# Kernel tuning notes

Hardware: AMD Instinct MI355X
Metric: run time of the kernel (lower is better)

## Reference

```python
import jax, jax.numpy as jnp
import numpy as np
import math

D_MODEL = 512
N_HEADS = 8
D_K = D_MODEL // N_HEADS
D_FF = 2048
EPS = 1e-6


def _layer_norm(x, gamma, beta):
    # Matches the torch module: unbiased std (ddof=1), divide by (std + eps)
    mean = jnp.mean(x, axis=-1, keepdims=True)
    std = jnp.std(x, axis=-1, ddof=1, keepdims=True)
    return gamma * (x - mean) / (std + EPS) + beta


def setup_inputs() -> dict:
    key = jax.random.key(0)
    ks = jax.random.split(key, 16)
    B, S = 4, 2048
    s_attn = 1.0 / math.sqrt(D_MODEL)
    s_ff1 = 1.0 / math.sqrt(D_MODEL)
    s_ff2 = 1.0 / math.sqrt(D_FF)
    inp = {
        "x": jax.random.normal(ks[0], (B, S, D_MODEL), dtype=jnp.float32),
        "mask": jnp.ones((1, 1, S, S), dtype=jnp.int32),
        "wq": jax.random.normal(ks[1], (D_MODEL, D_MODEL), jnp.float32) * s_attn,
        "bq": jnp.zeros((D_MODEL,), jnp.float32),
        "wk": jax.random.normal(ks[2], (D_MODEL, D_MODEL), jnp.float32) * s_attn,
        "bk": jnp.zeros((D_MODEL,), jnp.float32),
        "wv": jax.random.normal(ks[3], (D_MODEL, D_MODEL), jnp.float32) * s_attn,
        "bv": jnp.zeros((D_MODEL,), jnp.float32),
        "wo": jax.random.normal(ks[4], (D_MODEL, D_MODEL), jnp.float32) * s_attn,
        "bo": jnp.zeros((D_MODEL,), jnp.float32),
        "w1": jax.random.normal(ks[5], (D_MODEL, D_FF), jnp.float32) * s_ff1,
        "b1": jnp.zeros((D_FF,), jnp.float32),
        "w2": jax.random.normal(ks[6], (D_FF, D_MODEL), jnp.float32) * s_ff2,
        "b2": jnp.zeros((D_MODEL,), jnp.float32),
        "g1": jnp.ones((1, 1, D_MODEL), jnp.float32),
        "be1": jnp.zeros((1, 1, D_MODEL), jnp.float32),
        "g2": jnp.ones((1, 1, D_MODEL), jnp.float32),
        "be2": jnp.zeros((1, 1, D_MODEL), jnp.float32),
    }
    return inp


def reference(x, mask, wq, bq, wk, bk, wv, bv, wo, bo, w1, b1, w2, b2, g1, be1, g2, be2):
    B, S, _ = x.shape
    # --- residual 1: pre-norm self-attention ---
    xn = _layer_norm(x, g1, be1)
    q = (xn @ wq + bq).reshape(B, S, N_HEADS, D_K).transpose(0, 2, 1, 3)
    k = (xn @ wk + bk).reshape(B, S, N_HEADS, D_K).transpose(0, 2, 1, 3)
    v = (xn @ wv + bv).reshape(B, S, N_HEADS, D_K).transpose(0, 2, 1, 3)
    # NOTE: source uses floor division `//` by sqrt(d_k) (a faithful-ly kept bug)
    scores = jnp.floor_divide(jnp.einsum("bhqd,bhkd->bhqk", q, k), math.sqrt(D_K))
    scores = jnp.where(mask == 0, jnp.float32(-1e9), scores)
    attn = jax.nn.softmax(scores, axis=-1)
    ctx = jnp.einsum("bhqk,bhkd->bhqd", attn, v)
    ctx = ctx.transpose(0, 2, 1, 3).reshape(B, S, D_MODEL)
    x = x + (ctx @ wo + bo)
    # --- residual 2: pre-norm feed-forward ---
    xn2 = _layer_norm(x, g2, be2)
    ff = jax.nn.relu(xn2 @ w1 + b1) @ w2 + b2
    return x + ff
```

## Files before the change

### kernel.cpp

```cpp
#include <hip/hip_runtime.h>
#include <cmath>

#define SEQ 2048
#define DM 512
#define DFF 2048
#define NH 8
#define DKH 64
#define NROWS 8192

typedef __attribute__((ext_vector_type(8))) short bf16x8;
typedef __attribute__((ext_vector_type(16))) float f32x16;

__device__ __forceinline__ ushort f2bf(float f) {
    uint u = __float_as_uint(f);
    u += 0x7fff + ((u >> 16) & 1);
    return (ushort)(u >> 16);
}
__device__ __forceinline__ float bf2f(ushort h) {
    return __uint_as_float(((uint)h) << 16);
}
__device__ __forceinline__ uint cvtpk_bf16(float a, float b) {
    uint r;
    asm("v_cvt_pk_bf16_f32 %0, %1, %2" : "=v"(r) : "v"(a), "v"(b));
    return r;
}
__device__ __forceinline__ void gl_lds16(const void* g, void* l) {
    __builtin_amdgcn_global_load_lds(
        (const __attribute__((address_space(1))) void*)g,
        (__attribute__((address_space(3))) void*)l, 16, 0, 0);
}
__device__ __forceinline__ void* swz(char* base, int row, int col) {
    int byte = (row << 7) + (col << 1);
    byte ^= (row & 7) << 4;
    return base + byte;
}
__device__ __forceinline__ void* swzg(char* base, int row, int k) {
    int byte = (row << 7) + (k << 1);
    byte ^= ((row >> 2) & 7) << 4;
    return base + byte;
}

template<bool SPLIT>
__global__ __launch_bounds__(64) void ln_kernel(const float* __restrict__ x,
        const float* __restrict__ g, const float* __restrict__ b,
        ushort* __restrict__ oh, ushort* __restrict__ ol) {
    int row = blockIdx.x;
    int t = threadIdx.x;
    const float* xr = x + (size_t)row * DM + t * 8;
    float v[8];
    *(float4*)&v[0] = *(const float4*)(xr);
    *(float4*)&v[4] = *(const float4*)(xr + 4);
    float s = 0.f;
    #pragma unroll
    for (int j = 0; j < 8; ++j) s += v[j];
    #pragma unroll
    for (int m = 32; m > 0; m >>= 1) s += __shfl_xor(s, m);
    float mean = s * (1.0f / DM);
    float ss = 0.f;
    #pragma unroll
    for (int j = 0; j < 8; ++j) { float d = v[j] - mean; ss += d * d; }
    #pragma unroll
    for (int m = 32; m > 0; m >>= 1) ss += __shfl_xor(ss, m);
    float inv = 1.0f / (sqrtf(ss * (1.0f / (DM - 1))) + 1e-6f);
    float gv[8], bv[8];
    *(float4*)&gv[0] = *(const float4*)(g + t * 8);
    *(float4*)&gv[4] = *(const float4*)(g + t * 8 + 4);
    *(float4*)&bv[0] = *(const float4*)(b + t * 8);
    *(float4*)&bv[4] = *(const float4*)(b + t * 8 + 4);
    union { ushort us[8]; float4 f4; } ph, pl;
    #pragma unroll
    for (int j = 0; j < 8; ++j) {
        float o = gv[j] * (v[j] - mean) * inv + bv[j];
        ushort hb = f2bf(o);
        ph.us[j] = hb;
        if (SPLIT) pl.us[j] = f2bf(o - bf2f(hb));
    }
    *(float4*)(oh + (size_t)row * DM + t * 8) = ph.f4;
    if (SPLIT) *(float4*)(ol + (size_t)row * DM + t * 8) = pl.f4;
}

__global__ __launch_bounds__(256) void wconv4(
        const float* __restrict__ wq, const float* __restrict__ wk,
        const float* __restrict__ wv, const float* __restrict__ wo,
        ushort* __restrict__ qh, ushort* __restrict__ ql,
        ushort* __restrict__ kh, ushort* __restrict__ kl,
        ushort* __restrict__ vh, ushort* __restrict__ oh) {
    const int K = DM, N = DM;
    __shared__ float tile[64][65];
    int z = blockIdx.z;
    const float* W = (z == 0) ? wq : (z == 1) ? wk : (z == 2) ? wv : wo;
    ushort* Th = (z == 0) ? qh : (z == 1) ? kh : (z == 2) ? vh : oh;
    ushort* Tl = (z == 0) ? ql : (z == 1) ? kl : nullptr;
    bool split = (z < 2);
    int k0 = blockIdx.x * 64, n0 = blockIdx.y * 64;
    int t = threadIdx.x;
    {
        int kr = t >> 2, c0 = (t & 3) * 16;
        const float* src = W + (size_t)(k0 + kr) * N + n0 + c0;
        #pragma unroll
        for (int j = 0; j < 4; ++j)
            *(float4*)&tile[kr][c0 + j * 4] = *(const float4*)(src + j * 4);
    }
    __syncthreads();
    int n = t >> 2, kc = (t & 3) * 16;
    union { ushort us[16]; float4 f4[2]; } ph, pl;
    #pragma unroll
    for (int j = 0; j < 16; ++j) {
        float v = tile[kc + j][n];
        ushort hb = f2bf(v);
        ph.us[j] = hb;
        pl.us[j] = f2bf(v - bf2f(hb));
    }
    ushort* dh = Th + (size_t)(n0 + n) * K + k0 + kc;
    *(float4*)(dh) = ph.f4[0];
    *(float4*)(dh + 8) = ph.f4[1];
    if (split) {
        ushort* dl = Tl + (size_t)(n0 + n) * K + k0 + kc;
        *(float4*)(dl) = pl.f4[0];
        *(float4*)(dl + 8) = pl.f4[1];
    }
}

__global__ __launch_bounds__(256) void wconv(const float* __restrict__ W,
        ushort* __restrict__ Th, int K, int N) {
    __shared__ float tile[64][65];
    int k0 = blockIdx.x * 64, n0 = blockIdx.y * 64;
    int t = threadIdx.x;
    {
        int kr = t >> 2, c0 = (t & 3) * 16;
        const float* src = W + (size_t)(k0 + kr) * N + n0 + c0;
        #pragma unroll
        for (int j = 0; j < 4; ++j)
            *(float4*)&tile[kr][c0 + j * 4] = *(const float4*)(src + j * 4);
    }
    __syncthreads();
    int n = t >> 2, kc = (t & 3) * 16;
    union { ushort us[16]; float4 f4[2]; } ph;
    #pragma unroll
    for (int j = 0; j < 16; ++j) ph.us[j] = f2bf(tile[kc + j][n]);
    ushort* dh = Th + (size_t)(n0 + n) * K + k0 + kc;
    *(float4*)(dh) = ph.f4[0];
    *(float4*)(dh + 8) = ph.f4[1];
}

__global__ __launch_bounds__(256) void vtrans(const ushort* __restrict__ vh,
        ushort* __restrict__ vt) {
    __shared__ __align__(16) char tile[8192];
    int s0 = blockIdx.x * 64;
    int bh = blockIdx.y;
    int b = bh >> 3, h = bh & 7;
    int t = threadIdx.x;
    {
        int r = t >> 2, co = (t & 3) * 16;
        const ushort* src = vh + (size_t)(b * SEQ + s0 + r) * DM + h * DKH + co;
        *(float4*)swz(tile, r, co) = *(const float4*)(src);
        *(float4*)swz(tile, r, co + 8) = *(const float4*)(src + 8);
    }
    __syncthreads();
    int d = t >> 2, j0 = (t & 3) * 16;
    union { ushort us[16]; float4 f4[2]; } o;
    #pragma unroll
    for (int j = 0; j < 16; ++j)
        o.us[j] = *(ushort*)swz(tile, j0 + j, d);
    ushort* dst = vt + ((size_t)bh * DKH + d) * SEQ + s0 + j0;
    *(float4*)(dst) = o.f4[0];
    *(float4*)(dst + 8) = o.f4[1];
}

__global__ __launch_bounds__(64) void maskprep(const int* __restrict__ mask,
        ushort* __restrict__ mb, unsigned char* __restrict__ mflag) {
    int row = blockIdx.x;
    int lane = threadIdx.x;
    ushort neg = f2bf(-1e9f);
    unsigned long long bal[4];
    #pragma unroll
    for (int u = 0; u < 4; ++u) {
        int base = row * SEQ + u * 512 + lane * 8;
        int4 a = *(const int4*)(mask + base);
        int4 c = *(const int4*)(mask + base + 4);
        union { ushort us[8]; float4 f4; } o;
        o.us[0] = a.x ? (ushort)0 : neg;
        o.us[1] = a.y ? (ushort)0 : neg;
        o.us[2] = a.z ? (ushort)0 : neg;
        o.us[3] = a.w ? (ushort)0 : neg;
        o.us[4] = c.x ? (ushort)0 : neg;
        o.us[5] = c.y ? (ushort)0 : neg;
        o.us[6] = c.z ? (ushort)0 : neg;
        o.us[7] = c.w ? (ushort)0 : neg;
        *(float4*)(mb + base) = o.f4;
        bool ok = a.x && a.y && a.z && a.w && c.x && c.y && c.z && c.w;
        bal[u] = __ballot(ok);
    }
    if (lane < 32) {
        int u = lane >> 3;
        unsigned long long bsel = bal[0];
        bsel = (u == 1) ? bal[1] : bsel;
        bsel = (u == 2) ? bal[2] : bsel;
        bsel = (u == 3) ? bal[3] : bsel;
        int byte = (int)((bsel >> ((lane & 7) * 8)) & 0xFFull);
        mflag[row * 32 + lane] = (byte == 0xFF) ? 1 : 0;
    }
}

template<bool RELU, bool HASRES, int OUT>
__global__ __launch_bounds__(256) void mgemm(
        const ushort* __restrict__ Ah, const ushort* __restrict__ Bth,
        const float* __restrict__ bias, const float* __restrict__ resid,
        float* __restrict__ Cf, ushort* __restrict__ Cbh,
        int M, int N, int K) {
    __shared__ __align__(16) char smem[65536];
    int tid = threadIdx.x;
    int lane = tid & 63, w = tid >> 6;
    int ln31 = lane & 31, hi = lane >> 5;
    int mh = (w >> 1) * 64, nh = (w & 1) * 64;
    int gx = gridDim.x;
    int nwg = gx * gridDim.y;
    int flat = blockIdx.y * gx + blockIdx.x;
    int sid = (flat & 7) * (nwg >> 3) + (flat >> 3);
    int n0 = (sid % gx) * 128;
    int m0 = (sid / gx) * 128;

    f32x16 acc[2][2];
    #pragma unroll
    for (int i = 0; i < 2; ++i)
        #pragma unroll
        for (int j = 0; j < 2; ++j)
            #pragma unroll
            for (int r = 0; r < 16; ++r) acc[i][j][r] = 0.f;

    auto stage = [&](char* Abuf, char* Bbuf, int k0) {
        #pragma unroll
        for (int c = 0; c < 4; ++c) {
            int ch = w * 4 + c;
            int r = ch * 8 + (lane >> 3);
            int u = (lane & 7) ^ ((r >> 2) & 7);
            gl_lds16(Ah + (size_t)(m0 + r) * K + k0 + u * 8, Abuf + ch * 1024);
            gl_lds16(Bth + (size_t)(n0 + r) * K + k0 + u * 8, Bbuf + ch * 1024);
        }
    };

    char* A0 = smem;
    char* B0 = smem + 16384;
    char* A1 = smem + 32768;
    char* B1 = smem + 49152;

    stage(A0, B0, 0);
    __syncthreads();
    int nk = K / 64;
    for (int kt = 0; kt < nk; ++kt) {
        char* Ac = (kt & 1) ? A1 : A0;
        char* Bc = (kt & 1) ? B1 : B0;
        if (kt + 1 < nk)
            stage((kt & 1) ? A0 : A1, (kt & 1) ? B0 : B1, (kt + 1) * 64);
        __builtin_amdgcn_s_setprio(1);
        #pragma unroll
        for (int km = 0; km < 4; ++km) {
            int kk = km * 16 + hi * 8;
            bf16x8 ah[2], bh[2];
            ah[0] = *(bf16x8*)swzg(Ac, mh + ln31, kk);
            ah[1] = *(bf16x8*)swzg(Ac, mh + 32 + ln31, kk);
            bh[0] = *(bf16x8*)swzg(Bc, nh + ln31, kk);
            bh[1] = *(bf16x8*)swzg(Bc, nh + 32 + ln31, kk);
            #pragma unroll
            for (int mi = 0; mi < 2; ++mi)
                #pragma unroll
                for (int ni = 0; ni < 2; ++ni)
                    acc[mi][ni] = __builtin_amdgcn_mfma_f32_32x32x16_bf16(
                        ah[mi], bh[ni], acc[mi][ni], 0, 0, 0);
        }
        __builtin_amdgcn_s_setprio(0);
        __syncthreads();
    }
    float bv[2];
    bv[0] = bias[n0 + nh + ln31];
    bv[1] = bias[n0 + nh + 32 + ln31];
    #pragma unroll
    for (int mi = 0; mi < 2; ++mi)
        #pragma unroll
        for (int ni = 0; ni < 2; ++ni) {
            int n = n0 + nh + ni * 32 + ln31;
            #pragma unroll
            for (int r = 0; r < 16; ++r) {
                int m = m0 + mh + mi * 32 + (r & 3) + 8 * (r >> 2) + 4 * hi;
                float v = acc[mi][ni][r] + bv[ni];
                if (HASRES) v += resid[(size_t)m * N + n];
                if (RELU) v = fmaxf(v, 0.f);
                size_t idx = (size_t)m * N + n;
                if (OUT == 0) Cf[idx] = v;
                else Cbh[idx] = f2bf(v);
            }
        }
}

__global__ __launch_bounds__(256) void qkv_gemm(
        const ushort* __restrict__ Ah, const ushort* __restrict__ Al,
        const ushort* __restrict__ Bth, const ushort* __restrict__ Btl,
        const float* __restrict__ bq, const float* __restrict__ bk,
        const float* __restrict__ bv_, ushort* __restrict__ q_h,
        ushort* __restrict__ q_l, ushort* __restrict__ k_h,
        ushort* __restrict__ k_l, ushort* __restrict__ v_h) {
    const int K = DM, N = DM;
    __shared__ __align__(16) char smem[65536];
    char* As_h = smem;
    char* Bs_h = smem + 16384;
    char* As_l = smem + 32768;
    char* Bs_l = smem + 49152;
    int tid = threadIdx.x;
    int lane = tid & 63, w = tid >> 6;
    int ln31 = lane & 31, hi = lane >> 5;
    int mh = (w >> 1) * 64, nh = (w & 1) * 64;
    int gx = gridDim.x;
    int nwg = gx * gridDim.y;
    int flat = blockIdx.y * gx + blockIdx.x;
    int sid = (flat & 7) * (nwg >> 3) + (flat >> 3);
    int n0 = (sid % gx) * 128;
    int m0 = (sid / gx) * 128;
    bool isqk = (n0 < 1024);

    f32x16 acc[2][2];
    #pragma unroll
    for (int i = 0; i < 2; ++i)
        #pragma unroll
        for (int j = 0; j < 2; ++j)
            #pragma unroll
            for (int r = 0; r < 16; ++r) acc[i][j][r] = 0.f;

    for (int k0 = 0; k0 < K; k0 += 64) {
        #pragma unroll
        for (int c = 0; c < 4; ++c) {
            int ch = w * 4 + c;
            int r = ch * 8 + (lane >> 3);
            int u = (lane & 7) ^ ((r >> 2) & 7);
            gl_lds16(Ah + (size_t)(m0 + r) * K + k0 + u * 8, As_h + ch * 1024);
            gl_lds16(Bth + (size_t)(n0 + r) * K + k0 + u * 8, Bs_h + ch * 1024);
            if (isqk) {
                gl_lds16(Al + (size_t)(m0 + r) * K + k0 + u * 8, As_l + ch * 1024);
                gl_lds16(Btl + (size_t)(n0 + r) * K + k0 + u * 8, Bs_l + ch * 1024);
            }
        }
        __syncthreads();
        __builtin_amdgcn_s_setprio(1);
        #pragma unroll
        for (int km = 0; km < 4; ++km) {
            int kk = km * 16 + hi * 8;
            bf16x8 ah[2], bh[2];
            ah[0] = *(bf16x8*)swzg(As_h, mh + ln31, kk);
            ah[1] = *(bf16x8*)swzg(As_h, mh + 32 + ln31, kk);
            bh[0] = *(bf16x8*)swzg(Bs_h, nh + ln31, kk);
            bh[1] = *(bf16x8*)swzg(Bs_h, nh + 32 + ln31, kk);
            if (isqk) {
                bf16x8 al[2], bl[2];
                al[0] = *(bf16x8*)swzg(As_l, mh + ln31, kk);
                al[1] = *(bf16x8*)swzg(As_l, mh + 32 + ln31, kk);
                bl[0] = *(bf16x8*)swzg(Bs_l, nh + ln31, kk);
                bl[1] = *(bf16x8*)swzg(Bs_l, nh + 32 + ln31, kk);
                #pragma unroll
                for (int mi = 0; mi < 2; ++mi)
                    #pragma unroll
                    for (int ni = 0; ni < 2; ++ni) {
                        acc[mi][ni] = __builtin_amdgcn_mfma_f32_32x32x16_bf16(
                            ah[mi], bh[ni], acc[mi][ni], 0, 0, 0);
                        acc[mi][ni] = __builtin_amdgcn_mfma_f32_32x32x16_bf16(
                            ah[mi], bl[ni], acc[mi][ni], 0, 0, 0);
                        acc[mi][ni] = __builtin_amdgcn_mfma_f32_32x32x16_bf16(
                            al[mi], bh[ni], acc[mi][ni], 0, 0, 0);
                    }
            } else {
                #pragma unroll
                for (int mi = 0; mi < 2; ++mi)
                    #pragma unroll
                    for (int ni = 0; ni < 2; ++ni)
                        acc[mi][ni] = __builtin_amdgcn_mfma_f32_32x32x16_bf16(
                            ah[mi], bh[ni], acc[mi][ni], 0, 0, 0);
            }
        }
        __builtin_amdgcn_s_setprio(0);
        __syncthreads();
    }
    const float* bias = (n0 < 512) ? bq : (n0 < 1024 ? bk : bv_);
    int ncol0 = n0 & 511;
    ushort* Oh = (n0 < 512) ? q_h : (n0 < 1024 ? k_h : v_h);
    ushort* Ol = (n0 < 512) ? q_l : (n0 < 1024 ? k_l : nullptr);
    float bvv[2];
    bvv[0] = bias[ncol0 + nh + ln31];
    bvv[1] = bias[ncol0 + nh + 32 + ln31];
    #pragma unroll
    for (int mi = 0; mi < 2; ++mi)
        #pragma unroll
        for (int ni = 0; ni < 2; ++ni) {
            int n = ncol0 + nh + ni * 32 + ln31;
            #pragma unroll
            for (int r = 0; r < 16; ++r) {
                int m = m0 + mh + mi * 32 + (r & 3) + 8 * (r >> 2) + 4 * hi;
                float v = acc[mi][ni][r] + bvv[ni];
                size_t idx = (size_t)m * N + n;
                ushort hb = f2bf(v);
                Oh[idx] = hb;
                if (isqk) Ol[idx] = f2bf(v - bf2f(hb));
            }
        }
}

__global__ __launch_bounds__(256, 3) void attn_kernel(
        const ushort* __restrict__ Qh, const ushort* __restrict__ Ql,
        const ushort* __restrict__ Khg, const ushort* __restrict__ Klg,
        const ushort* __restrict__ Vtg, const ushort* __restrict__ mb,
        const unsigned char* __restrict__ mflag,
        ushort* __restrict__ pctx0, ushort* __restrict__ pctx1,
        float2* __restrict__ ml) {
    __shared__ __align__(16) char smem[49152];
    int tid = threadIdx.x;
    int w = tid >> 6, lane = tid & 63;
    int ln31 = lane & 31, hi = lane >> 5;
    bool hib = (hi != 0);
    int f = blockIdx.y * gridDim.x + blockIdx.x;
    int g = (f & 7) * 128 + (f >> 3);
    int bh = g >> 5, rest = g & 31;
    int part = rest >> 4, qb = rest & 15;
    int b = bh >> 3, h = bh & 7;
    int q0 = qb * 128;
    size_t brow = (size_t)b * SEQ;
    int hcol = h * DKH;
    int ktbeg = part * 16, ktend = ktbeg + 16;

    auto stage_kv = [&](char* buf, int kt) {
        #pragma unroll
        for (int c = 0; c < 2; ++c) {
            int ch = w * 2 + c;
            int r = ch * 8 + (lane >> 3);
            int u = (lane & 7) ^ (r & 7);
            gl_lds16(Khg + (brow + kt * 64 + r) * DM + hcol + u * 8,
                     buf + ch * 1024);
            gl_lds16(Klg + (brow + kt * 64 + r) * DM + hcol + u * 8,
                     buf + 8192 + ch * 1024);
            gl_lds16(Vtg + ((size_t)bh * DKH + r) * SEQ + kt * 64 + u * 8,
                     buf + 16384 + ch * 1024);
        }
    };

    {
        char* QhL = smem;
        char* QlL = smem + 16384;
        #pragma unroll
        for (int c = 0; c < 4; ++c) {
            int ch = w * 4 + c;
            int r = ch * 8 + (lane >> 3);
            int u = (lane & 7) ^ (r & 7);
            gl_lds16(Qh + (brow + q0 + r) * DM + hcol + u * 8, QhL + ch * 1024);
            gl_lds16(Ql + (brow + q0 + r) * DM + hcol + u * 8, QlL + ch * 1024);
        }
    }
    __syncthreads();
    bf16x8 qfh[4], qfl[4];
    {
        int qr = w * 32 + ln31;
        #pragma unroll
        for (int c = 0; c < 4; ++c) {
            qfh[c] = *(bf16x8*)swz(smem, qr, c * 16 + hi * 8);
            qfl[c] = *(bf16x8*)swz(smem + 16384, qr, c * 16 + hi * 8);
        }
    }
    __syncthreads();
    stage_kv(smem + (ktbeg & 1) * 24576, ktbeg);
    __syncthreads();

    f32x16 ctx0, ctx1;
    #pragma unroll
    for (int r = 0; r < 16; ++r) { ctx0[r] = 0.f; ctx1[r] = 0.f; }
    float m_i = -1e30f, l_i = 0.f;
    int qglob = q0 + w * 32 + ln31;
    const ushort* mrow = mb + (size_t)qglob * SEQ;

    for (int kt = ktbeg; kt < ktend; ++kt) {
        char* cur = smem + (kt & 1) * 24576;
        if (kt + 1 < ktend)
            stage_kv(smem + ((kt + 1) & 1) * 24576, kt + 1);
        unsigned char fl = mflag[qglob * 32 + kt];
        bool domask = !__all(fl != 0);
        ushort4 mpre[8];
        if (domask) {
            #pragma unroll
            for (int i = 0; i < 8; ++i)
                mpre[i] = *(const ushort4*)(mrow + kt * 64 + i * 8 + hi * 4);
        }
        char* KhL = cur;
        char* KlL = cur + 8192;
        char* VtL = cur + 16384;
        #pragma unroll
        for (int ksub = 0; ksub < 2; ++ksub) {
            f32x16 s;
            #pragma unroll
            for (int r = 0; r < 16; ++r) s[r] = 0.f;
            __builtin_amdgcn_s_setprio(1);
            #pragma unroll
            for (int c = 0; c < 4; ++c) {
                bf16x8 ka = *(bf16x8*)swz(KhL, ksub * 32 + ln31, c * 16 + hi * 8);
                bf16x8 kb = *(bf16x8*)swz(KlL, ksub * 32 + ln31, c * 16 + hi * 8);
                s = __builtin_amdgcn_mfma_f32_32x32x16_bf16(ka, qfh[c], s, 0, 0, 0);
                s = __builtin_amdgcn_mfma_f32_32x32x16_bf16(ka, qfl[c], s, 0, 0, 0);
                s = __builtin_amdgcn_mfma_f32_32x32x16_bf16(kb, qfh[c], s, 0, 0, 0);
            }
            __builtin_amdgcn_s_setprio(0);
            float tmax = -1e30f;
            if (domask) {
                #pragma unroll
                for (int rg = 0; rg < 4; ++rg) {
                    ushort4 mv = mpre[ksub * 4 + rg];
                    ushort mu[4] = {mv.x, mv.y, mv.z, mv.w};
                    #pragma unroll
                    for (int j = 0; j < 4; ++j) {
                        int r = rg * 4 + j;
                        float sc = floorf(s[r] * 0.125f) + bf2f(mu[j]);
                        s[r] = sc;
                        tmax = fmaxf(tmax, sc);
                    }
                }
            } else {
                #pragma unroll
                for (int r = 0; r < 16; ++r) {
                    float sc = floorf(s[r] * 0.125f);
                    s[r] = sc;
                    tmax = fmaxf(tmax, sc);
                }
            }
            tmax = fmaxf(tmax, __shfl_xor(tmax, 32));
            if (!__all(tmax <= m_i)) {
                float newm = fmaxf(m_i, tmax);
                float scl = __expf(m_i - newm);
                m_i = newm;
                l_i *= scl;
                #pragma unroll
                for (int r = 0; r < 16; ++r) { ctx0[r] *= scl; ctx1[r] *= scl; }
            }
            float psum = 0.f;
            #pragma unroll
            for (int r = 0; r < 16; ++r) {
                float p = __expf(s[r] - m_i);
                s[r] = p;
                psum += p;
            }
            psum += __shfl_xor(psum, 32);
            l_i += psum;
            uint pk0[4], pk1[4];
            #pragma unroll
            for (int rg = 0; rg < 4; ++rg) {
                pk0[rg] = cvtpk_bf16(s[rg * 4 + 0], s[rg * 4 + 1]);
                pk1[rg] = cvtpk_bf16(s[rg * 4 + 2], s[rg * 4 + 3]);
            }
            __builtin_amdgcn_s_setprio(1);
            #pragma unroll
            for (int cc = 0; cc < 2; ++cc) {
                uint A0 = pk0[cc * 2], A1 = pk1[cc * 2];
                uint B0 = pk0[cc * 2 + 1], B1 = pk1[cc * 2 + 1];
                uint send0 = hib ? A0 : B0;
                uint send1 = hib ? A1 : B1;
                uint own0  = hib ? B0 : A0;
                uint own1  = hib ? B1 : A1;
                uint recv0 = (uint)__shfl_xor((int)send0, 32);
                uint recv1 = (uint)__shfl_xor((int)send1, 32);
                union { uint u[4]; bf16x8 v; } pb;
                pb.u[0] = hib ? recv0 : own0;
                pb.u[1] = hib ? recv1 : own1;
                pb.u[2] = hib ? own0 : recv0;
                pb.u[3] = hib ? own1 : recv1;
                int c = ksub * 2 + cc;
                bf16x8 va0 = *(bf16x8*)swz(VtL, ln31, c * 16 + hi * 8);
                bf16x8 va1 = *(bf16x8*)swz(VtL, 32 + ln31, c * 16 + hi * 8);
                ctx0 = __builtin_amdgcn_mfma_f32_32x32x16_bf16(va0, pb.v, ctx0, 0, 0, 0);
                ctx1 = __builtin_amdgcn_mfma_f32_32x32x16_bf16(va1, pb.v, ctx1, 0, 0, 0);
            }
            __builtin_amdgcn_s_setprio(0);
        }
        __syncthreads();
    }

    ushort* P = part ? pctx1 : pctx0;
    size_t pbase = ((size_t)bh * SEQ + qglob) * DKH;
    #pragma unroll
    for (int r = 0; r < 16; ++r) {
        int d = (r & 3) + 8 * (r >> 2) + 4 * hi;
        P[pbase + d] = f2bf(ctx0[r]);
        P[pbase + 32 + d] = f2bf(ctx1[r]);
    }
    if (hi == 0)
        ml[((size_t)part * 32 + bh) * SEQ + qglob] = make_float2(m_i, l_i);
}

__global__ __launch_bounds__(256) void attn_combine(
        const ushort* __restrict__ p0, const ushort* __restrict__ p1,
        const float2* __restrict__ ml, ushort* __restrict__ O) {
    int idx = blockIdx.x * 256 + threadIdx.x;
    int d0 = (idx & 7) * 8;
    int q = (idx >> 3) & (SEQ - 1);
    int bh = idx >> 14;
    int b = bh >> 3, h = bh & 7;
    size_t pb = ((size_t)bh * SEQ + q) * DKH + d0;
    bf16x8 c0 = *(const bf16x8*)(p0 + pb);
    bf16x8 c1 = *(const bf16x8*)(p1 + pb);
    float2 e0 = ml[(size_t)bh * SEQ + q];
    float2 e1 = ml[((size_t)32 + bh) * SEQ + q];
    float m = fmaxf(e0.x, e1.x);
    float w0 = __expf(e0.x - m), w1 = __expf(e1.x - m);
    float inv = 1.0f / (e0.y * w0 + e1.y * w1);
    union { ushort us[8]; float4 f4; } o;
    #pragma unroll
    for (int j = 0; j < 8; ++j) {
        float v0 = bf2f((ushort)c0[j]);
        float v1 = bf2f((ushort)c1[j]);
        o.us[j] = f2bf((v0 * w0 + v1 * w1) * inv);
    }
    *(float4*)(O + ((size_t)(b * SEQ + q)) * DM + h * DKH + d0) = o.f4;
}

extern "C" void kernel_launch(void* const* d_in, const int* in_sizes, int n_in,
                              void* d_out, int out_size, void* d_ws, size_t ws_size,
                              hipStream_t stream) {
    const float* x    = (const float*)d_in[0];
    const int*   mask = (const int*)d_in[1];
    const float* wq = (const float*)d_in[2];
    const float* bq = (const float*)d_in[3];
    const float* wk = (const float*)d_in[4];
    const float* bk = (const float*)d_in[5];
    const float* wv = (const float*)d_in[6];
    const float* bv = (const float*)d_in[7];
    const float* wo = (const float*)d_in[8];
    const float* bo = (const float*)d_in[9];
    const float* w1 = (const float*)d_in[10];
    const float* b1 = (const float*)d_in[11];
    const float* w2 = (const float*)d_in[12];
    const float* b2 = (const float*)d_in[13];
    const float* g1  = (const float*)d_in[14];
    const float* be1 = (const float*)d_in[15];
    const float* g2  = (const float*)d_in[16];
    const float* be2 = (const float*)d_in[17];
    float* out = (float*)d_out;

    char* ws = (char*)d_ws;
    const size_t MiB = 1024 * 1024;
    ushort* xn_h = (ushort*)(ws);
    ushort* xn_l = (ushort*)(ws + 8 * MiB);
    ushort* q_h  = (ushort*)(ws + 16 * MiB);
    ushort* q_l  = (ushort*)(ws + 24 * MiB);
    ushort* k_h  = (ushort*)(ws + 32 * MiB);
    ushort* k_l  = (ushort*)(ws + 40 * MiB);
    ushort* v_h  = (ushort*)(ws + 48 * MiB);
    ushort* v_t  = (ushort*)(ws + 56 * MiB);
    ushort* wqkvt_h = (ushort*)(ws + 64 * MiB);
    ushort* wqkvt_l = (ushort*)(ws + 66 * MiB);
    ushort* wot_h = (ushort*)(ws + 67 * MiB);
    unsigned char* mflag = (unsigned char*)(ws + 67 * MiB + 512 * 1024);
    ushort* w1t_h = (ushort*)(ws + 68 * MiB);
    ushort* w2t_h = (ushort*)(ws + 70 * MiB);
    ushort* mb    = (ushort*)(ws + 72 * MiB);
    ushort* pctx0 = (ushort*)(ws + 80 * MiB);
    ushort* pctx1 = (ushort*)(ws + 88 * MiB);
    float2* ml    = (float2*)(ws + 64 * MiB);
    ushort* ctx  = xn_h;
    ushort* xn2  = xn_l;
    ushort* ff1  = q_h;

    dim3 blk256(256);
    wconv4<<<dim3(8, 8, 4), blk256, 0, stream>>>(
        wq, wk, wv, wo, wqkvt_h, wqkvt_l, wqkvt_h + 512 * 512,
        wqkvt_l + 512 * 512, wqkvt_h + 1024 * 512, wot_h);
    wconv<<<dim3(8, 32), blk256, 0, stream>>>(w1, w1t_h, DM, DFF);
    wconv<<<dim3(32, 8), blk256, 0, stream>>>(w2, w2t_h, DFF, DM);
    maskprep<<<SEQ, 64, 0, stream>>>(mask, mb, mflag);
    ln_kernel<true><<<NROWS, 64, 0, stream>>>(x, g1, be1, xn_h, xn_l);
    qkv_gemm<<<dim3(12, NROWS / 128), blk256, 0, stream>>>(
        xn_h, xn_l, wqkvt_h, wqkvt_l, bq, bk, bv, q_h, q_l, k_h, k_l, v_h);
    vtrans<<<dim3(SEQ / 64, 4 * NH), blk256, 0, stream>>>(v_h, v_t);
    {
        dim3 grid(32, 32);
        attn_kernel<<<grid, blk256, 0, stream>>>(
            q_h, q_l, k_h, k_l, v_t, mb, mflag, pctx0, pctx1, ml);
    }
    attn_combine<<<32 * SEQ * 8 / 256, blk256, 0, stream>>>(pctx0, pctx1, ml, ctx);
    {
        dim3 grid(DM / 128, NROWS / 128);
        mgemm<false,true,0><<<grid, blk256, 0, stream>>>(
            ctx, wot_h, bo, x, out, nullptr, NROWS, DM, DM);
    }
    ln_kernel<false><<<NROWS, 64, 0, stream>>>(out, g2, be2, xn2, nullptr);
    {
        dim3 grid(DFF / 128, NROWS / 128);
        mgemm<true,false,1><<<grid, blk256, 0, stream>>>(
            xn2, w1t_h, b1, nullptr, nullptr, ff1, NROWS, DFF, DM);
    }
    {
        dim3 grid(DM / 128, NROWS / 128);
        mgemm<false,true,0><<<grid, blk256, 0, stream>>>(
            ff1, w2t_h, b2, out, out, nullptr, NROWS, DM, DFF);
    }
}
```

Baseline: 238.2 us.

## Single-buffer V, widen QK tile, and fold score scale into Q projection

```diff
diff --git a/kernel.cpp b/kernel.cpp
--- a/kernel.cpp
+++ b/kernel.cpp
@@ -381,6 +381,7 @@
     int ncol0 = n0 & 511;
     ushort* Oh = (n0 < 512) ? q_h : (n0 < 1024 ? k_h : v_h);
     ushort* Ol = (n0 < 512) ? q_l : (n0 < 1024 ? k_l : nullptr);
+    float scale = (n0 < 512) ? 0.125f : 1.0f;
     float bvv[2];
     bvv[0] = bias[ncol0 + nh + ln31];
     bvv[1] = bias[ncol0 + nh + 32 + ln31];
@@ -392,7 +393,7 @@
             #pragma unroll
             for (int r = 0; r < 16; ++r) {
                 int m = m0 + mh + mi * 32 + (r & 3) + 8 * (r >> 2) + 4 * hi;
-                float v = acc[mi][ni][r] + bvv[ni];
+                float v = (acc[mi][ni][r] + bvv[ni]) * scale;
                 size_t idx = (size_t)m * N + n;
                 ushort hb = f2bf(v);
                 Oh[idx] = hb;
@@ -401,14 +402,14 @@
         }
 }
 
-__global__ __launch_bounds__(256, 3) void attn_kernel(
+__global__ __launch_bounds__(256, 4) void attn_kernel(
         const ushort* __restrict__ Qh, const ushort* __restrict__ Ql,
         const ushort* __restrict__ Khg, const ushort* __restrict__ Klg,
         const ushort* __restrict__ Vtg, const ushort* __restrict__ mb,
         const unsigned char* __restrict__ mflag,
         ushort* __restrict__ pctx0, ushort* __restrict__ pctx1,
         float2* __restrict__ ml) {
-    __shared__ __align__(16) char smem[49152];
+    __shared__ __align__(16) char smem[40960];
     int tid = threadIdx.x;
     int w = tid >> 6, lane = tid & 63;
     int ln31 = lane & 31, hi = lane >> 5;
@@ -423,7 +424,8 @@
     int hcol = h * DKH;
     int ktbeg = part * 16, ktend = ktbeg + 16;
 
-    auto stage_kv = [&](char* buf, int kt) {
+    auto stage_K = [&](int kt) {
+        char* buf = smem + (kt & 1) * 16384;
         #pragma unroll
         for (int c = 0; c < 2; ++c) {
             int ch = w * 2 + c;
@@ -433,8 +435,17 @@
                      buf + ch * 1024);
             gl_lds16(Klg + (brow + kt * 64 + r) * DM + hcol + u * 8,
                      buf + 8192 + ch * 1024);
+        }
+    };
+    auto stage_V = [&](int kt) {
+        char* buf = smem + 32768;
+        #pragma unroll
+        for (int c = 0; c < 2; ++c) {
+            int ch = w * 2 + c;
+            int r = ch * 8 + (lane >> 3);
+            int u = (lane & 7) ^ (r & 7);
             gl_lds16(Vtg + ((size_t)bh * DKH + r) * SEQ + kt * 64 + u * 8,
-                     buf + 16384 + ch * 1024);
+                     buf + ch * 1024);
         }
     };
 
@@ -461,7 +472,8 @@
         }
     }
     __syncthreads();
-    stage_kv(smem + (ktbeg & 1) * 24576, ktbeg);
+    stage_K(ktbeg);
+    stage_V(ktbeg);
     __syncthreads();
 
     f32x16 ctx0, ctx1;
@@ -472,82 +484,87 @@
     const ushort* mrow = mb + (size_t)qglob * SEQ;
 
     for (int kt = ktbeg; kt < ktend; ++kt) {
-        char* cur = smem + (kt & 1) * 24576;
-        if (kt + 1 < ktend)
-            stage_kv(smem + ((kt + 1) & 1) * 24576, kt + 1);
+        if (kt + 1 < ktend) stage_K(kt + 1);
+        char* KhL = smem + (kt & 1) * 16384;
+        char* KlL = KhL + 8192;
+        char* VtL = smem + 32768;
         unsigned char fl = mflag[qglob * 32 + kt];
         bool domask = !__all(fl != 0);
-        ushort4 mpre[8];
+
+        f32x16 s0, s1;
+        #pragma unroll
+        for (int r = 0; r < 16; ++r) { s0[r] = 0.f; s1[r] = 0.f; }
+        __builtin_amdgcn_s_setprio(1);
+        #pragma unroll
+        for (int c = 0; c < 4; ++c) {
+            bf16x8 ka0 = *(bf16x8*)swz(KhL, ln31, c * 16 + hi * 8);
+            bf16x8 kb0 = *(bf16x8*)swz(KlL, ln31, c * 16 + hi * 8);
+            bf16x8 ka1 = *(bf16x8*)swz(KhL, 32 + ln31, c * 16 + hi * 8);
+            bf16x8 kb1 = *(bf16x8*)swz(KlL, 32 + ln31, c * 16 + hi * 8);
+            s0 = __builtin_amdgcn_mfma_f32_32x32x16_bf16(ka0, qfh[c], s0, 0, 0, 0);
+            s1 = __builtin_amdgcn_mfma_f32_32x32x16_bf16(ka1, qfh[c], s1, 0, 0, 0);
+            s0 = __builtin_amdgcn_mfma_f32_32x32x16_bf16(ka0, qfl[c], s0, 0, 0, 0);
+            s1 = __builtin_amdgcn_mfma_f32_32x32x16_bf16(ka1, qfl[c], s1, 0, 0, 0);
+            s0 = __builtin_amdgcn_mfma_f32_32x32x16_bf16(kb0, qfh[c], s0, 0, 0, 0);
+            s1 = __builtin_amdgcn_mfma_f32_32x32x16_bf16(kb1, qfh[c], s1, 0, 0, 0);
+        }
+        __builtin_amdgcn_s_setprio(0);
+
         if (domask) {
             #pragma unroll
-            for (int i = 0; i < 8; ++i)
-                mpre[i] = *(const ushort4*)(mrow + kt * 64 + i * 8 + hi * 4);
-        }
-        char* KhL = cur;
-        char* KlL = cur + 8192;
-        char* VtL = cur + 16384;
-        #pragma unroll
-        for (int ksub = 0; ksub < 2; ++ksub) {
-            f32x16 s;
-            #pragma unroll
-            for (int r = 0; r < 16; ++r) s[r] = 0.f;
-            __builtin_amdgcn_s_setprio(1);
-            #pragma unroll
-            for (int c = 0; c < 4; ++c) {
-                bf16x8 ka = *(bf16x8*)swz(KhL, ksub * 32 + ln31, c * 16 + hi * 8);
-                bf16x8 kb = *(bf16x8*)swz(KlL, ksub * 32 + ln31, c * 16 + hi * 8);
-                s = __builtin_amdgcn_mfma_f32_32x32x16_bf16(ka, qfh[c], s, 0, 0, 0);
-                s = __builtin_amdgcn_mfma_f32_32x32x16_bf16(ka, qfl[c], s, 0, 0, 0);
-                s = __builtin_amdgcn_mfma_f32_32x32x16_bf16(kb, qfh[c], s, 0, 0, 0);
-            }
-            __builtin_amdgcn_s_setprio(0);
-            float tmax = -1e30f;
-            if (domask) {
+            for (int rg = 0; rg < 4; ++rg) {
+                ushort4 mv0 = *(const ushort4*)(mrow + kt * 64 + rg * 8 + hi * 4);
+                ushort4 mv1 = *(const ushort4*)(mrow + kt * 64 + 32 + rg * 8 + hi * 4);
+                ushort mu0[4] = {mv0.x, mv0.y, mv0.z, mv0.w};
+                ushort mu1[4] = {mv1.x, mv1.y, mv1.z, mv1.w};
                 #pragma unroll
-                for (int rg = 0; rg < 4; ++rg) {
-                    ushort4 mv = mpre[ksub * 4 + rg];
-                    ushort mu[4] = {mv.x, mv.y, mv.z, mv.w};
-                    #pragma unroll
-                    for (int j = 0; j < 4; ++j) {
-                        int r = rg * 4 + j;
-                        float sc = floorf(s[r] * 0.125f) + bf2f(mu[j]);
-                        s[r] = sc;
-                        tmax = fmaxf(tmax, sc);
-                    }
-                }
-            } else {
-                #pragma unroll
-                for (int r = 0; r < 16; ++r) {
-                    float sc = floorf(s[r] * 0.125f);
-                    s[r] = sc;
-                    tmax = fmaxf(tmax, sc);
+                for (int j = 0; j < 4; ++j) {
+                    s0[rg * 4 + j] = floorf(s0[rg * 4 + j]) + bf2f(mu0[j]);
+                    s1[rg * 4 + j] = floorf(s1[rg * 4 + j]) + bf2f(mu1[j]);
                 }
             }
-            tmax = fmaxf(tmax, __shfl_xor(tmax, 32));
-            if (!__all(tmax <= m_i)) {
-                float newm = fmaxf(m_i, tmax);
-                float scl = __expf(m_i - newm);
-                m_i = newm;
-                l_i *= scl;
-                #pragma unroll
-                for (int r = 0; r < 16; ++r) { ctx0[r] *= scl; ctx1[r] *= scl; }
+        } else {
+            #pragma unroll
+            for (int r = 0; r < 16; ++r) {
+                s0[r] = floorf(s0[r]);
+                s1[r] = floorf(s1[r]);
             }
-            float psum = 0.f;
-            #pragma unroll
-            for (int r = 0; r < 16; ++r) {
-                float p = __expf(s[r] - m_i);
-                s[r] = p;
-                psum += p;
+        }
+        float tmax = -1e30f;
+        #pragma unroll
+        for (int r = 0; r < 16; ++r)
+            tmax = fmaxf(tmax, fmaxf(s0[r], s1[r]));
+        tmax = fmaxf(tmax, __shfl_xor(tmax, 32));
+        if (!__all(tmax <= m_i)) {
+            float newm = fmaxf(m_i, tmax);
+            float scl = __expf(m_i - newm);
+            m_i = newm;
+            l_i *= scl;
+            #pragma unroll
+            for (int r = 0; r < 16; ++r) { ctx0[r] *= scl; ctx1[r] *= scl; }
+        }
+        float psum = 0.f;
+        #pragma unroll
+        for (int r = 0; r < 16; ++r) {
+            float p0 = __expf(s0[r] - m_i);
+            float p1 = __expf(s1[r] - m_i);
+            s0[r] = p0;
+            s1[r] = p1;
+            psum += p0 + p1;
+        }
+        psum += __shfl_xor(psum, 32);
+        l_i += psum;
+
+        bf16x8 pb[4];
+        #pragma unroll
+        for (int ksub = 0; ksub < 2; ++ksub) {
+            uint pk0[4], pk1[4];
+            #pragma unroll
+            for (int rg = 0; rg < 4; ++rg) {
+                const f32x16& sv = ksub ? s1 : s0;
+                pk0[rg] = cvtpk_bf16(sv[rg * 4 + 0], sv[rg * 4 + 1]);
+                pk1[rg] = cvtpk_bf16(sv[rg * 4 + 2], sv[rg * 4 + 3]);
             }
-            psum += __shfl_xor(psum, 32);
-            l_i += psum;
-            uint pk0[4], pk1[4];
-            #pragma unroll
-            for (int rg = 0; rg < 4; ++rg) {
-                pk0[rg] = cvtpk_bf16(s[rg * 4 + 0], s[rg * 4 + 1]);
-                pk1[rg] = cvtpk_bf16(s[rg * 4 + 2], s[rg * 4 + 3]);
-            }
-            __builtin_amdgcn_s_setprio(1);
             #pragma unroll
             for (int cc = 0; cc < 2; ++cc) {
                 uint A0 = pk0[cc * 2], A1 = pk1[cc * 2];
@@ -558,20 +575,27 @@
                 uint own1  = hib ? B1 : A1;
                 uint recv0 = (uint)__shfl_xor((int)send0, 32);
                 uint recv1 = (uint)__shfl_xor((int)send1, 32);
-                union { uint u[4]; bf16x8 v; } pb;
-                pb.u[0] = hib ? recv0 : own0;
-                pb.u[1] = hib ? recv1 : own1;
-                pb.u[2] = hib ? own0 : recv0;
-                pb.u[3] = hib ? own1 : recv1;
-                int c = ksub * 2 + cc;
-                bf16x8 va0 = *(bf16x8*)swz(VtL, ln31, c * 16 + hi * 8);
-                bf16x8 va1 = *(bf16x8*)swz(VtL, 32 + ln31, c * 16 + hi * 8);
-                ctx0 = __builtin_amdgcn_mfma_f32_32x32x16_bf16(va0, pb.v, ctx0, 0, 0, 0);
-                ctx1 = __builtin_amdgcn_mfma_f32_32x32x16_bf16(va1, pb.v, ctx1, 0, 0, 0);
+                union { uint u[4]; bf16x8 v; } pbu;
+                pbu.u[0] = hib ? recv0 : own0;
+                pbu.u[1] = hib ? recv1 : own1;
+                pbu.u[2] = hib ? own0 : recv0;
+                pbu.u[3] = hib ? own1 : recv1;
+                pb[ksub * 2 + cc] = pbu.v;
             }
-            __builtin_amdgcn_s_setprio(0);
-        }
+        }
+
         __syncthreads();
+        __builtin_amdgcn_s_setprio(1);
+        #pragma unroll
+        for (int c = 0; c < 4; ++c) {
+            bf16x8 va0 = *(bf16x8*)swz(VtL, ln31, c * 16 + hi * 8);
+            bf16x8 va1 = *(bf16x8*)swz(VtL, 32 + ln31, c * 16 + hi * 8);
+            ctx0 = __builtin_amdgcn_mfma_f32_32x32x16_bf16(va0, pb[c], ctx0, 0, 0, 0);
+            ctx1 = __builtin_amdgcn_mfma_f32_32x32x16_bf16(va1, pb[c], ctx1, 0, 0, 0);
+        }
+        __builtin_amdgcn_s_setprio(0);
+        __syncthreads();
+        if (kt + 1 < ktend) stage_V(kt + 1);
     }
 
     ushort* P = part ? pctx1 : pctx0;
```

New measurement: 357.4 us. 1.5x slower.

## Fold score scale into Q projection and single-buffer V to shrink attention LDS

Applied to the files above, without the earlier changes.

```diff
diff --git a/kernel.cpp b/kernel.cpp
--- a/kernel.cpp
+++ b/kernel.cpp
@@ -381,6 +381,7 @@
     int ncol0 = n0 & 511;
     ushort* Oh = (n0 < 512) ? q_h : (n0 < 1024 ? k_h : v_h);
     ushort* Ol = (n0 < 512) ? q_l : (n0 < 1024 ? k_l : nullptr);
+    float scale = (n0 < 512) ? 0.125f : 1.0f;
     float bvv[2];
     bvv[0] = bias[ncol0 + nh + ln31];
     bvv[1] = bias[ncol0 + nh + 32 + ln31];
@@ -392,7 +393,7 @@
             #pragma unroll
             for (int r = 0; r < 16; ++r) {
                 int m = m0 + mh + mi * 32 + (r & 3) + 8 * (r >> 2) + 4 * hi;
-                float v = acc[mi][ni][r] + bvv[ni];
+                float v = (acc[mi][ni][r] + bvv[ni]) * scale;
                 size_t idx = (size_t)m * N + n;
                 ushort hb = f2bf(v);
                 Oh[idx] = hb;
@@ -408,7 +409,7 @@
         const unsigned char* __restrict__ mflag,
         ushort* __restrict__ pctx0, ushort* __restrict__ pctx1,
         float2* __restrict__ ml) {
-    __shared__ __align__(16) char smem[49152];
+    __shared__ __align__(16) char smem[40960];
     int tid = threadIdx.x;
     int w = tid >> 6, lane = tid & 63;
     int ln31 = lane & 31, hi = lane >> 5;
@@ -423,7 +424,8 @@
     int hcol = h * DKH;
     int ktbeg = part * 16, ktend = ktbeg + 16;
 
-    auto stage_kv = [&](char* buf, int kt) {
+    auto stage_K = [&](int kt) {
+        char* buf = smem + (kt & 1) * 16384;
         #pragma unroll
         for (int c = 0; c < 2; ++c) {
             int ch = w * 2 + c;
@@ -433,8 +435,17 @@
                      buf + ch * 1024);
             gl_lds16(Klg + (brow + kt * 64 + r) * DM + hcol + u * 8,
                      buf + 8192 + ch * 1024);
+        }
+    };
+    auto stage_V = [&](int kt) {
+        char* buf = smem + 32768;
+        #pragma unroll
+        for (int c = 0; c < 2; ++c) {
+            int ch = w * 2 + c;
+            int r = ch * 8 + (lane >> 3);
+            int u = (lane & 7) ^ (r & 7);
             gl_lds16(Vtg + ((size_t)bh * DKH + r) * SEQ + kt * 64 + u * 8,
-                     buf + 16384 + ch * 1024);
+                     buf + ch * 1024);
         }
     };
 
@@ -461,7 +472,8 @@
         }
     }
     __syncthreads();
-    stage_kv(smem + (ktbeg & 1) * 24576, ktbeg);
+    stage_K(ktbeg);
+    stage_V(ktbeg);
     __syncthreads();
 
     f32x16 ctx0, ctx1;
@@ -472,9 +484,10 @@
     const ushort* mrow = mb + (size_t)qglob * SEQ;
 
     for (int kt = ktbeg; kt < ktend; ++kt) {
-        char* cur = smem + (kt & 1) * 24576;
-        if (kt + 1 < ktend)
-            stage_kv(smem + ((kt + 1) & 1) * 24576, kt + 1);
+        if (kt + 1 < ktend) stage_K(kt + 1);
+        char* KhL = smem + (kt & 1) * 16384;
+        char* KlL = KhL + 8192;
+        char* VtL = smem + 32768;
         unsigned char fl = mflag[qglob * 32 + kt];
         bool domask = !__all(fl != 0);
         ushort4 mpre[8];
@@ -483,9 +496,6 @@
             for (int i = 0; i < 8; ++i)
                 mpre[i] = *(const ushort4*)(mrow + kt * 64 + i * 8 + hi * 4);
         }
-        char* KhL = cur;
-        char* KlL = cur + 8192;
-        char* VtL = cur + 16384;
         #pragma unroll
         for (int ksub = 0; ksub < 2; ++ksub) {
             f32x16 s;
@@ -510,7 +520,7 @@
                     #pragma unroll
                     for (int j = 0; j < 4; ++j) {
                         int r = rg * 4 + j;
-                        float sc = floorf(s[r] * 0.125f) + bf2f(mu[j]);
+                        float sc = floorf(s[r]) + bf2f(mu[j]);
                         s[r] = sc;
                         tmax = fmaxf(tmax, sc);
                     }
@@ -518,7 +528,7 @@
             } else {
                 #pragma unroll
                 for (int r = 0; r < 16; ++r) {
-                    float sc = floorf(s[r] * 0.125f);
+                    float sc = floorf(s[r]);
                     s[r] = sc;
                     tmax = fmaxf(tmax, sc);
                 }
@@ -547,7 +557,7 @@
                 pk0[rg] = cvtpk_bf16(s[rg * 4 + 0], s[rg * 4 + 1]);
                 pk1[rg] = cvtpk_bf16(s[rg * 4 + 2], s[rg * 4 + 3]);
             }
-            __builtin_amdgcn_s_setprio(1);
+            bf16x8 pb[2];
             #pragma unroll
             for (int cc = 0; cc < 2; ++cc) {
                 uint A0 = pk0[cc * 2], A1 = pk1[cc * 2];
@@ -558,20 +568,27 @@
                 uint own1  = hib ? B1 : A1;
                 uint recv0 = (uint)__shfl_xor((int)send0, 32);
                 uint recv1 = (uint)__shfl_xor((int)send1, 32);
-                union { uint u[4]; bf16x8 v; } pb;
-                pb.u[0] = hib ? recv0 : own0;
-                pb.u[1] = hib ? recv1 : own1;
-                pb.u[2] = hib ? own0 : recv0;
-                pb.u[3] = hib ? own1 : recv1;
+                union { uint u[4]; bf16x8 v; } pbu;
+                pbu.u[0] = hib ? recv0 : own0;
+                pbu.u[1] = hib ? recv1 : own1;
+                pbu.u[2] = hib ? own0 : recv0;
+                pbu.u[3] = hib ? own1 : recv1;
+                pb[cc] = pbu.v;
+            }
+            if (ksub == 0) __syncthreads();
+            __builtin_amdgcn_s_setprio(1);
+            #pragma unroll
+            for (int cc = 0; cc < 2; ++cc) {
                 int c = ksub * 2 + cc;
                 bf16x8 va0 = *(bf16x8*)swz(VtL, ln31, c * 16 + hi * 8);
                 bf16x8 va1 = *(bf16x8*)swz(VtL, 32 + ln31, c * 16 + hi * 8);
-                ctx0 = __builtin_amdgcn_mfma_f32_32x32x16_bf16(va0, pb.v, ctx0, 0, 0, 0);
-                ctx1 = __builtin_amdgcn_mfma_f32_32x32x16_bf16(va1, pb.v, ctx1, 0, 0, 0);
+                ctx0 = __builtin_amdgcn_mfma_f32_32x32x16_bf16(va0, pb[cc], ctx0, 0, 0, 0);
+                ctx1 = __builtin_amdgcn_mfma_f32_32x32x16_bf16(va1, pb[cc], ctx1, 0, 0, 0);
             }
             __builtin_amdgcn_s_setprio(0);
         }
         __syncthreads();
+        if (kt + 1 < ktend) stage_V(kt + 1);
     }
 
     ushort* P = part ? pctx1 : pctx0;
```

Result: slower. 247.9 us (+4.1%).
